# Kernel tuning notes

Hardware: AMD Instinct MI355X
Metric: run time of the kernel (lower is better)

Reference implementation:

```python
import jax, jax.numpy as jnp
import numpy as np

B, H, W, C = 32, 64, 64, 512
NUM_HEADS = 16
WS = 8          # window_size
SHIFT = 4       # shift_size = WS // 2
MLP_HIDDEN = 2048
N = WS * WS     # tokens per window
NW = (H // WS) * (W // WS)  # windows per image


def _rel_coords_table():
    # Swin-V2 log-spaced continuous relative coordinates, (1, 2*WS-1, 2*WS-1, 2)
    r = np.arange(-(WS - 1), WS, dtype=np.float32)
    t = np.stack(np.meshgrid(r, r, indexing='ij'), axis=-1)[None]
    t = t / (WS - 1) * 8.0
    t = np.sign(t) * np.log2(np.abs(t) + 1.0) / np.log2(8.0)
    return t.astype(np.float32)


def _rel_pos_index():
    coords = np.stack(np.meshgrid(np.arange(WS), np.arange(WS), indexing='ij'))
    cf = coords.reshape(2, -1)
    rel = (cf[:, :, None] - cf[:, None, :]).transpose(1, 2, 0)
    rel[..., 0] += WS - 1
    rel[..., 1] += WS - 1
    rel[..., 0] *= 2 * WS - 1
    return rel.sum(-1)  # (N, N) int


def _attn_mask():
    # shifted-window mask: -100 where tokens come from different image regions
    img = np.zeros((H, W), np.float32)
    cnt = 0
    for hs in (slice(0, -WS), slice(-WS, -SHIFT), slice(-SHIFT, None)):
        for ws_ in (slice(0, -WS), slice(-WS, -SHIFT), slice(-SHIFT, None)):
            img[hs, ws_] = cnt
            cnt += 1
    mw = img.reshape(H // WS, WS, W // WS, WS).transpose(0, 2, 1, 3).reshape(-1, N)
    diff = mw[:, None, :] - mw[:, :, None]
    return np.where(diff != 0, np.float32(-100.0), np.float32(0.0))  # (NW, N, N)


_RCT = jnp.asarray(_rel_coords_table())
_RPI = jnp.asarray(_rel_pos_index().reshape(-1))
_MASK = jnp.asarray(_attn_mask())
_LOGIT_MAX = float(np.log(1.0 / 0.01))


def _layernorm(x, w, b):
    mu = x.mean(-1, keepdims=True)
    var = ((x - mu) ** 2).mean(-1, keepdims=True)
    return (x - mu) / jnp.sqrt(var + 1e-5) * w + b


def setup_inputs() -> dict:
    key = jax.random.key(0)
    ks = jax.random.split(key, 8)
    s = 0.02
    return {
        'x': jax.random.normal(ks[0], (B, H * W, C), jnp.float32),
        'qkv_w': jax.random.normal(ks[1], (3 * C, C), jnp.float32) * s,
        'q_bias': jnp.zeros((C,), jnp.float32),
        'v_bias': jnp.zeros((C,), jnp.float32),
        'logit_scale': jnp.log(10.0 * jnp.ones((NUM_HEADS, 1, 1), jnp.float32)),
        'cpb_w1': jax.random.normal(ks[2], (512, 2), jnp.float32) * s,
        'cpb_b1': jnp.zeros((512,), jnp.float32),
        'cpb_w2': jax.random.normal(ks[3], (NUM_HEADS, 512), jnp.float32) * s,
        'proj_w': jax.random.normal(ks[4], (C, C), jnp.float32) * s,
        'proj_b': jnp.zeros((C,), jnp.float32),
        'norm1_w': jnp.ones((C,), jnp.float32),
        'norm1_b': jnp.zeros((C,), jnp.float32),
        'norm2_w': jnp.ones((C,), jnp.float32),
        'norm2_b': jnp.zeros((C,), jnp.float32),
        'fc1_w': jax.random.normal(ks[5], (MLP_HIDDEN, C), jnp.float32) * s,
        'fc1_b': jnp.zeros((MLP_HIDDEN,), jnp.float32),
        'fc2_w': jax.random.normal(ks[6], (C, MLP_HIDDEN), jnp.float32) * s,
        'fc2_b': jnp.zeros((C,), jnp.float32),
    }


def reference(x, qkv_w, q_bias, v_bias, logit_scale, cpb_w1, cpb_b1, cpb_w2,
              proj_w, proj_b, norm1_w, norm1_b, norm2_w, norm2_b,
              fc1_w, fc1_b, fc2_w, fc2_b):
    hd = C // NUM_HEADS
    shortcut = x
    xi = x.reshape(B, H, W, C)
    xi = jnp.roll(xi, shift=(-SHIFT, -SHIFT), axis=(1, 2))
    # window partition -> (B*NW, N, C)
    xw = xi.reshape(B, H // WS, WS, W // WS, WS, C).transpose(0, 1, 3, 2, 4, 5).reshape(-1, N, C)
    # qkv with q/v bias only (k bias = 0), Swin-V2 style
    qkv_b = jnp.concatenate([q_bias, jnp.zeros_like(v_bias), v_bias])
    qkv = (xw @ qkv_w.T + qkv_b).reshape(-1, N, 3, NUM_HEADS, hd).transpose(2, 0, 3, 1, 4)
    q, k, v = qkv[0], qkv[1], qkv[2]  # (B_, nH, N, hd)
    # cosine attention
    qn = q / jnp.maximum(jnp.linalg.norm(q, axis=-1, keepdims=True), 1e-12)
    kn = k / jnp.maximum(jnp.linalg.norm(k, axis=-1, keepdims=True), 1e-12)
    attn = jnp.einsum('whnd,whmd->whnm', qn, kn)
    scale = jnp.exp(jnp.minimum(logit_scale, _LOGIT_MAX))  # (nH,1,1)
    attn = attn * scale
    # continuous relative position bias via small MLP
    table = (jax.nn.relu(_RCT @ cpb_w1.T + cpb_b1) @ cpb_w2.T).reshape(-1, NUM_HEADS)
    bias = table[_RPI].reshape(N, N, NUM_HEADS).transpose(2, 0, 1)  # (nH, N, N)
    bias = 16.0 * jax.nn.sigmoid(bias)
    attn = attn + bias[None]
    # shift mask
    attn = attn.reshape(B, NW, NUM_HEADS, N, N) + _MASK[None, :, None]
    attn = jax.nn.softmax(attn.reshape(-1, NUM_HEADS, N, N), axis=-1)
    out = jnp.einsum('whnm,whmd->whnd', attn, v).transpose(0, 2, 1, 3).reshape(-1, N, C)
    out = out @ proj_w.T + proj_b
    # window reverse + un-shift
    xi = out.reshape(B, H // WS, W // WS, WS, WS, C).transpose(0, 1, 3, 2, 4, 5).reshape(B, H, W, C)
    xi = jnp.roll(xi, shift=(SHIFT, SHIFT), axis=(1, 2)).reshape(B, H * W, C)
    # Swin-V2 post-norm residuals
    x = shortcut + _layernorm(xi, norm1_w, norm1_b)
    h = jax.nn.gelu(x @ fc1_w.T + fc1_b, approximate=False)
    y = h @ fc2_w.T + fc2_b
    x = x + _layernorm(y, norm2_w, norm2_b)
    return x
```

## Files before the change

kernel.cpp:

```cpp
#include <hip/hip_runtime.h>

typedef unsigned short u16;
typedef unsigned int u32;
typedef __attribute__((ext_vector_type(8))) __bf16 bf16x8;
typedef __attribute__((ext_vector_type(8))) short s16x8;
typedef __attribute__((ext_vector_type(4))) short s16x4;
typedef __attribute__((ext_vector_type(4))) float f32x4;

static __device__ __forceinline__ float bf2f(u16 h){
  union{u32 u; float f;} v; v.u = ((u32)h)<<16; return v.f;
}
static __device__ __forceinline__ u16 cvtbf(float f){
  return __builtin_bit_cast(u16, (__bf16)f);
}

#define GLD16(gp, lp) __builtin_amdgcn_global_load_lds(                      \
  (__attribute__((address_space(1))) void*)(void*)(gp),                      \
  (__attribute__((address_space(3))) void*)(void*)(lp), 16, 0, 0)

__global__ __launch_bounds__(256)
void prep_x_kernel(const float* __restrict__ x, u16* __restrict__ xw)
{
  const int t = threadIdx.x, wv = t>>6, ln = t&63;
  const size_t row = (size_t)blockIdx.x*4 + wv;
  const int b = (int)(row>>12), wl = (int)((row>>6)&63), m = (int)(row&63);
  const int gh = ((wl>>3)*8 + (m>>3) + 4) & 63;
  const int gw = ((wl&7)*8 + (m&7) + 4) & 63;
  const size_t src = ((size_t)b*4096 + (size_t)gh*64 + gw)*512 + (size_t)ln*8;
  f32x4 a = *(const f32x4*)&x[src];
  f32x4 c = *(const f32x4*)&x[src+4];
  s16x8 o;
#pragma unroll
  for (int j=0;j<4;j++){ o[j] = (short)cvtbf(a[j]); o[j+4] = (short)cvtbf(c[j]); }
  *(s16x8*)&xw[row*512 + (size_t)ln*8] = o;
}

__global__ __launch_bounds__(256)
void cvt_bf16_kernel(const float* __restrict__ src, u16* __restrict__ dst, int n)
{
  const int i = (blockIdx.x*256 + threadIdx.x)*8;
  if (i >= n) return;
  f32x4 a = *(const f32x4*)&src[i];
  f32x4 c = *(const f32x4*)&src[i+4];
  s16x8 o;
#pragma unroll
  for (int j=0;j<4;j++){ o[j] = (short)cvtbf(a[j]); o[j+4] = (short)cvtbf(c[j]); }
  *(s16x8*)&dst[i] = o;
}

static __device__ __forceinline__ float logcoord(int d){
  const float tt = (float)d * (8.0f/7.0f);
  const float sg = (tt > 0.f) ? 1.f : ((tt < 0.f) ? -1.f : 0.f);
  return sg * log2f(fabsf(tt) + 1.f) * (1.f/3.f);
}

__global__ __launch_bounds__(512)
void cpb_table_kernel(const float* __restrict__ w1, const float* __restrict__ b1,
                      const float* __restrict__ w2, float* __restrict__ table)
{
  __shared__ float hid[512];
  const int r = blockIdx.x, j = threadIdx.x;
  const float va = logcoord(r/15 - 7);
  const float vb = logcoord(r%15 - 7);
  hid[j] = fmaxf(va*w1[2*j] + vb*w1[2*j+1] + b1[j], 0.f);
  __syncthreads();
  if (j < 16){
    float acc = 0.f;
    for (int i=0;i<512;i++) acc += hid[i]*w2[j*512+i];
    table[r*16 + j] = acc;
  }
}

__global__ __launch_bounds__(256)
void bias_expand_kernel(const float* __restrict__ table, float* __restrict__ biasT)
{
  const int gid = blockIdx.x*256 + threadIdx.x;
  const int h = gid>>12, ij = gid&4095, i = ij>>6, j = ij&63;
  const int dr = (i>>3)-(j>>3)+7, dc = (i&7)-(j&7)+7;
  const float v = table[(dr*15+dc)*16 + h];
  biasT[gid] = 16.f / (1.f + __expf(-v));
}

template<int EPI>
__global__ __launch_bounds__(512, 4)
void gemm128(const u16* __restrict__ A, const u16* __restrict__ B,
             u16* __restrict__ Co, const float* __restrict__ bias0,
             const float* __restrict__ bias1, int N, int K)
{
  extern __shared__ u16 ls[];
  const int t = threadIdx.x;
  const int wv = t>>6, ln = t&63;
  const int wr = wv>>2, wc = wv&3;
  const int lr = ln&15, lg = ln>>4;
  const int gx = gridDim.x;
  const int lin = blockIdx.y*gx + blockIdx.x;
  const int q = (gx*(int)gridDim.y)>>3;
  const int lin2 = (lin&7)*q + (lin>>3);
  const int mT = lin2/gx, nT = lin2 - mT*gx;

  const int rSub = ln>>2;
  const int cS = ((ln&3) ^ ((ln>>3)&3)) * 8;
  const u16* gA = A + (size_t)(mT*128 + wv*16 + rSub)*K + cS;
  const u16* gB = B + (size_t)(nT*256 + wv*16 + rSub)*K + cS;
  const size_t rstepB = (size_t)128*K;
  char* lA = (char*)ls + wv*1024;

  const int cR = (lg ^ ((lr>>1)&3))*8;
  const int offA0 = (wr*64 + lr)*32 + cR;
  const int offB0 = (wc*64 + lr)*32 + cR;

#define STAGE(buf, tt) do {                                                  \
    char* p_ = lA + (buf)*24576;                                             \
    const size_t ko_ = (size_t)(tt)*32;                                      \
    GLD16(gA + ko_,          p_);                                            \
    GLD16(gB + ko_,          p_ + 8192);                                     \
    GLD16(gB + ko_ + rstepB, p_ + 16384);                                    \
  } while(0)

  f32x4 acc[4][4] = {};

#define COMPUTE(buf) do {                                                    \
    const u16* la_ = ls + (buf)*12288;                                       \
    const u16* lb_ = la_ + 4096;                                             \
    bf16x8 bfr[4];                                                           \
    _Pragma("unroll")                                                        \
    for (int nt=0;nt<4;nt++) bfr[nt] = *(const bf16x8*)&lb_[offB0 + nt*512]; \
    _Pragma("unroll")                                                        \
    for (int mt=0;mt<4;mt++){                                                \
      bf16x8 af = *(const bf16x8*)&la_[offA0 + mt*512];                      \
      _Pragma("unroll")                                                      \
      for (int nt=0;nt<4;nt++)                                               \
        acc[mt][nt] = __builtin_amdgcn_mfma_f32_16x16x32_bf16(af, bfr[nt], acc[mt][nt], 0,0,0); \
    }                                                                        \
  } while(0)

  const int nsteps = K>>5;
  STAGE(0,0); STAGE(1,1);
  int cb = 0;
  for (int t_=0; t_<nsteps-1; ++t_){
    asm volatile("s_waitcnt vmcnt(3)\n\ts_barrier" ::: "memory");
    if (t_+2 < nsteps){
      int sb = cb+2; if (sb>=3) sb-=3;
      STAGE(sb, t_+2);
    }
    COMPUTE(cb);
    cb = (cb==2)?0:cb+1;
  }
  asm volatile("s_waitcnt vmcnt(0)\n\ts_barrier" ::: "memory");
  COMPUTE(cb);
#undef STAGE
#undef COMPUTE

  if (EPI == 0) {
    const int cb0 = nT*256 + wc*64;
    int secA[4], hhA[4], dA[4]; float bbA[4];
#pragma unroll
    for (int nt=0; nt<4; nt++) {
      const int cbp = cb0 + nt*16;
      secA[nt] = cbp >> 9;
      hhA[nt]  = (cbp >> 5) & 15;
      dA[nt]   = (cbp & 16) + lr;
      bbA[nt]  = (secA[nt]==1) ? 0.f : ((secA[nt]==0)?bias0:bias1)[(hhA[nt]<<5)+dA[nt]];
    }
#pragma unroll
    for (int mt=0; mt<4; mt++) {
      const int row = mT*128 + wr*64 + mt*16 + lg*4;
      const int win = row>>6, tok0 = row&63;
#pragma unroll
      for (int rr=0; rr<4; rr++) {
#pragma unroll
        for (int nt=0; nt<4; nt++) {
          u16* p = Co + (size_t)secA[nt]*67108864ULL + (size_t)win*32768
                      + hhA[nt]*2048 + (tok0+rr)*32 + dA[nt];
          *p = cvtbf(acc[mt][nt][rr] + bbA[nt]);
        }
      }
    }
  } else {
    const int c0 = nT*256 + wc*64;
    const int r0 = mT*128 + wr*64 + lg*4;
    float bbA[4];
#pragma unroll
    for (int nt=0; nt<4; nt++) bbA[nt] = bias0[c0 + nt*16 + lr];
#pragma unroll
    for (int mt=0; mt<4; mt++) {
#pragma unroll
      for (int rr=0; rr<4; rr++) {
        u16* pr = Co + (size_t)(r0 + mt*16 + rr)*N + c0 + lr;
#pragma unroll
        for (int nt=0; nt<4; nt++) {
          float v = acc[mt][nt][rr] + bbA[nt];
          if (EPI == 2) {
            const float z = 1.5957691216f * v * fmaf(0.044715f, v*v, 1.0f);
            v = v * __builtin_amdgcn_rcpf(1.0f + __expf(-z));
          }
          pr[nt*16] = cvtbf(v);
        }
      }
    }
  }
}

__global__ __launch_bounds__(256)
void attn_win(const u16* __restrict__ qkv, const float* __restrict__ biasT,
              const float* __restrict__ logit_scale, u16* __restrict__ aout)
{
  __shared__ float sb[4096];
  __shared__ u16 sp[4][4096];
  __shared__ u16 svt[4][2048];
  const int t = threadIdx.x, wv = t>>6, ln = t&63;
  const int lr = ln&15, lg = ln>>4;
  const int head = blockIdx.y;
  for (int i = t; i < 4096; i += 256) sb[i] = biasT[head*4096 + i];
  __syncthreads();
  const int win = blockIdx.x*4 + wv;
  const size_t whi = (size_t)win*16 + head;
  const u16* qb = qkv + whi*2048;
  const u16* kb = qkv + 67108864ULL + whi*2048;
  const u16* vb = qkv + 134217728ULL + whi*2048;

  s16x8 qs[4], ks[4];
  float qin[4], kin[4];
#pragma unroll
  for (int mt=0;mt<4;mt++){
    qs[mt] = *(const s16x8*)&qb[(mt*16+lr)*32 + lg*8];
    float ss = 0.f;
#pragma unroll
    for (int j=0;j<8;j++){ float f = bf2f((u16)qs[mt][j]); ss += f*f; }
    ss += __shfl_xor(ss, 16); ss += __shfl_xor(ss, 32);
    qin[mt] = 1.f / fmaxf(sqrtf(ss), 1e-12f);
  }
#pragma unroll
  for (int nt=0;nt<4;nt++){
    ks[nt] = *(const s16x8*)&kb[(nt*16+lr)*32 + lg*8];
    float ss = 0.f;
#pragma unroll
    for (int j=0;j<8;j++){ float f = bf2f((u16)ks[nt][j]); ss += f*f; }
    ss += __shfl_xor(ss, 16); ss += __shfl_xor(ss, 32);
    kin[nt] = 1.f / fmaxf(sqrtf(ss), 1e-12f);
  }
  f32x4 S[4][4] = {};
#pragma unroll
  for (int mt=0;mt<4;mt++)
#pragma unroll
    for (int nt=0;nt<4;nt++)
      S[mt][nt] = __builtin_amdgcn_mfma_f32_16x16x32_bf16(
          __builtin_bit_cast(bf16x8, qs[mt]), __builtin_bit_cast(bf16x8, ks[nt]),
          S[mt][nt], 0,0,0);

  const float scale = expf(fminf(logit_scale[head], 4.6051702f));
  const int wl = win & 63, wh = wl>>3, ww = wl&7;
  float rsum[4][4];
#pragma unroll
  for (int mt=0;mt<4;mt++){
#pragma unroll
    for (int rr=0;rr<4;rr++){
      const int msub = lg*4 + rr;
      const float qn = __shfl(qin[mt], msub);
      const int m = mt*16 + msub;
      const int ridm = (wh==7 ? (((m>>3)<4) ? 3 : 6) : 0) + (ww==7 ? (((m&7)<4) ? 1 : 2) : 0);
#pragma unroll
      for (int nt=0;nt<4;nt++){
        const int n = nt*16 + lr;
        const int ridn = (wh==7 ? (((n>>3)<4) ? 3 : 6) : 0) + (ww==7 ? (((n&7)<4) ? 1 : 2) : 0);
        float v = S[mt][nt][rr] * (qn * kin[nt] * scale) + sb[m*64+n];
        if (ridm != ridn) v -= 100.f;
        S[mt][nt][rr] = v;
      }
      float mx = fmaxf(fmaxf(S[mt][0][rr], S[mt][1][rr]), fmaxf(S[mt][2][rr], S[mt][3][rr]));
      mx = fmaxf(mx, __shfl_xor(mx, 1)); mx = fmaxf(mx, __shfl_xor(mx, 2));
      mx = fmaxf(mx, __shfl_xor(mx, 4)); mx = fmaxf(mx, __shfl_xor(mx, 8));
      float sm = 0.f;
#pragma unroll
      for (int nt=0;nt<4;nt++){ float p = __expf(S[mt][nt][rr]-mx); S[mt][nt][rr] = p; sm += p; }
      sm += __shfl_xor(sm,1); sm += __shfl_xor(sm,2); sm += __shfl_xor(sm,4); sm += __shfl_xor(sm,8);
      rsum[mt][rr] = sm;
#pragma unroll
      for (int nt=0;nt<4;nt++){
        const int n = nt*16 + lr;
        sp[wv][(m*64 + n) ^ ((m&7)<<3)] = cvtbf(S[mt][nt][rr]);
      }
    }
  }
#pragma unroll
  for (int it=0; it<8; it++){
    const int flat = it*256 + ln*4;
    const int k = flat>>5, d0 = flat&31;
    s16x4 vv = *(const s16x4*)&vb[k*32 + d0];
#pragma unroll
    for (int e=0;e<4;e++)
      svt[wv][((d0+e)*64 + k) ^ (((d0+e)&7)<<3)] = (u16)vv[e];
  }
  f32x4 O[4][2] = {};
#pragma unroll
  for (int kk=0; kk<2; kk++){
    bf16x8 pf[4], vf[2];
#pragma unroll
    for (int mt=0;mt<4;mt++){
      const int am = mt*16 + lr;
      const int idx = (am*64 + kk*32 + lg*8) ^ ((am&7)<<3);
      s16x8 tmp; __builtin_memcpy(&tmp, (const char*)&sp[wv][0] + 2*idx, 16);
      pf[mt] = __builtin_bit_cast(bf16x8, tmp);
    }
#pragma unroll
    for (int n2=0;n2<2;n2++){
      const int vn = n2*16 + lr;
      const int idx = (vn*64 + kk*32 + lg*8) ^ ((vn&7)<<3);
      s16x8 tmp; __builtin_memcpy(&tmp, (const char*)&svt[wv][0] + 2*idx, 16);
      vf[n2] = __builtin_bit_cast(bf16x8, tmp);
    }
#pragma unroll
    for (int mt=0;mt<4;mt++)
#pragma unroll
      for (int n2=0;n2<2;n2++)
        O[mt][n2] = __builtin_amdgcn_mfma_f32_16x16x32_bf16(pf[mt], vf[n2], O[mt][n2], 0,0,0);
  }
  const size_t obase = (size_t)win*64;
#pragma unroll
  for (int mt=0;mt<4;mt++)
#pragma unroll
  for (int rr=0;rr<4;rr++){
    const int m = mt*16 + lg*4 + rr;
    const float inv = 1.f / rsum[mt][rr];
#pragma unroll
    for (int n2=0;n2<2;n2++){
      const int d = n2*16 + lr;
      aout[(obase + m)*512 + head*32 + d] = cvtbf(O[mt][n2][rr] * inv);
    }
  }
}

__global__ __launch_bounds__(256)
void scatter_ln_kernel(const u16* __restrict__ po, const float* __restrict__ x,
                       const float* __restrict__ w, const float* __restrict__ bb,
                       u16* __restrict__ x1b)
{
  const int t = threadIdx.x, wv = t>>6, ln = t&63;
  const size_t row = (size_t)blockIdx.x*4 + wv;
  s16x8 pv = *(const s16x8*)&po[row*512 + (size_t)ln*8];
  float v[8]; float s=0.f, s2=0.f;
#pragma unroll
  for (int j=0;j<8;j++){ v[j] = bf2f((u16)pv[j]); s += v[j]; s2 += v[j]*v[j]; }
#pragma unroll
  for (int d=1; d<64; d<<=1){ s += __shfl_xor(s,d); s2 += __shfl_xor(s2,d); }
  const float mu = s * 0.001953125f;
  const float var = s2 * 0.001953125f - mu*mu;
  const float rs = rsqrtf(var + 1e-5f);
  const int b = (int)(row>>12), wl = (int)((row>>6)&63), m = (int)(row&63);
  const int gh = ((wl>>3)*8 + (m>>3) + 4) & 63;
  const int gw = ((wl&7)*8 + (m&7) + 4) & 63;
  const size_t img = ((size_t)b*4096 + (size_t)gh*64 + gw)*512 + (size_t)ln*8;
  f32x4 xa = *(const f32x4*)&x[img];
  f32x4 xc = *(const f32x4*)&x[img+4];
  s16x8 ob;
  const int c0 = ln*8;
#pragma unroll
  for (int j=0;j<8;j++){
    const int c = c0 + j;
    const float lnv = (v[j]-mu)*rs*w[c] + bb[c];
    const float xx = (j<4) ? xa[j] : xc[j-4];
    ob[j] = (short)cvtbf(xx + lnv);
  }
  *(s16x8*)&x1b[img] = ob;
}

__global__ __launch_bounds__(256)
void final_ln_kernel(const u16* __restrict__ y, const u16* __restrict__ x1b,
                     const float* __restrict__ w, const float* __restrict__ bb,
                     float* __restrict__ out)
{
  const int t = threadIdx.x, wv = t>>6, ln = t&63;
  const size_t row = (size_t)blockIdx.x*4 + wv;
  const size_t idx = row*512 + (size_t)ln*8;
  s16x8 yv = *(const s16x8*)&y[idx];
  float v[8]; float s=0.f, s2=0.f;
#pragma unroll
  for (int j=0;j<8;j++){ v[j] = bf2f((u16)yv[j]); s += v[j]; s2 += v[j]*v[j]; }
#pragma unroll
  for (int d=1; d<64; d<<=1){ s += __shfl_xor(s,d); s2 += __shfl_xor(s2,d); }
  const float mu = s * 0.001953125f;
  const float var = s2 * 0.001953125f - mu*mu;
  const float rs = rsqrtf(var + 1e-5f);
  s16x8 xv = *(const s16x8*)&x1b[idx];
  f32x4 oa, oc;
  const int c0 = ln*8;
#pragma unroll
  for (int j=0;j<8;j++){
    const int c = c0 + j;
    const float lnv = (v[j]-mu)*rs*w[c] + bb[c];
    const float o = bf2f((u16)xv[j]) + lnv;
    if (j<4) oa[j] = o; else oc[j-4] = o;
  }
  *(f32x4*)&out[idx] = oa;
  *(f32x4*)&out[idx+4] = oc;
}

extern "C" void kernel_launch(void* const* d_in, const int* in_sizes, int n_in,
                              void* d_out, int out_size, void* d_ws, size_t ws_size,
                              hipStream_t stream)
{
  (void)in_sizes; (void)n_in; (void)out_size; (void)ws_size;
  const float* x        = (const float*)d_in[0];
  const float* qkv_w    = (const float*)d_in[1];
  const float* q_bias   = (const float*)d_in[2];
  const float* v_bias   = (const float*)d_in[3];
  const float* lscale   = (const float*)d_in[4];
  const float* cpb_w1   = (const float*)d_in[5];
  const float* cpb_b1   = (const float*)d_in[6];
  const float* cpb_w2   = (const float*)d_in[7];
  const float* proj_w   = (const float*)d_in[8];
  const float* proj_b   = (const float*)d_in[9];
  const float* n1w      = (const float*)d_in[10];
  const float* n1b      = (const float*)d_in[11];
  const float* n2w      = (const float*)d_in[12];
  const float* n2b      = (const float*)d_in[13];
  const float* fc1_w    = (const float*)d_in[14];
  const float* fc1_b    = (const float*)d_in[15];
  const float* fc2_w    = (const float*)d_in[16];
  const float* fc2_b    = (const float*)d_in[17];

  char* ws = (char*)d_ws;
  constexpr size_t XW_OFF   = 0;
  constexpr size_t ATT_OFF  = 134217728ULL;
  constexpr size_t PRJ_OFF  = 268435456ULL;
  constexpr size_t H_OFF    = 0;
  constexpr size_t BIAS_OFF = 536870912ULL;
  constexpr size_t TAB_OFF  = BIAS_OFF + 262144;
  constexpr size_t WQKV_OFF = TAB_OFF + 16384;
  constexpr size_t WPRJ_OFF = WQKV_OFF + 1572864;
  constexpr size_t WFC1_OFF = WPRJ_OFF + 524288;
  constexpr size_t WFC2_OFF = WFC1_OFF + 2097152;
  constexpr size_t QKV_OFF  = WFC2_OFF + 2097152;
  constexpr size_t X1B_OFF  = QKV_OFF;
  constexpr size_t Y_OFF    = QKV_OFF + 134217728ULL;

  u16*   xw    = (u16*)(ws + XW_OFF);
  u16*   attnO = (u16*)(ws + ATT_OFF);
  u16*   projO = (u16*)(ws + PRJ_OFF);
  u16*   hbuf  = (u16*)(ws + H_OFF);
  float* biasT = (float*)(ws + BIAS_OFF);
  float* table = (float*)(ws + TAB_OFF);
  u16*   wqkv  = (u16*)(ws + WQKV_OFF);
  u16*   wprj  = (u16*)(ws + WPRJ_OFF);
  u16*   wfc1  = (u16*)(ws + WFC1_OFF);
  u16*   wfc2  = (u16*)(ws + WFC2_OFF);
  u16*   qkvB  = (u16*)(ws + QKV_OFF);
  u16*   x1b   = (u16*)(ws + X1B_OFF);
  u16*   ybuf  = (u16*)(ws + Y_OFF);

  hipFuncSetAttribute((const void*)gemm128<0>, hipFuncAttributeMaxDynamicSharedMemorySize, 73728);
  hipFuncSetAttribute((const void*)gemm128<1>, hipFuncAttributeMaxDynamicSharedMemorySize, 73728);
  hipFuncSetAttribute((const void*)gemm128<2>, hipFuncAttributeMaxDynamicSharedMemorySize, 73728);
  hipFuncSetAttribute((const void*)gemm128<3>, hipFuncAttributeMaxDynamicSharedMemorySize, 73728);

  cvt_bf16_kernel<<<384, 256, 0, stream>>>(qkv_w, wqkv, 786432);
  cvt_bf16_kernel<<<128, 256, 0, stream>>>(proj_w, wprj, 262144);
  cvt_bf16_kernel<<<512, 256, 0, stream>>>(fc1_w, wfc1, 1048576);
  cvt_bf16_kernel<<<512, 256, 0, stream>>>(fc2_w, wfc2, 1048576);
  prep_x_kernel<<<32768, 256, 0, stream>>>(x, xw);
  cpb_table_kernel<<<225, 512, 0, stream>>>(cpb_w1, cpb_b1, cpb_w2, table);
  bias_expand_kernel<<<256, 256, 0, stream>>>(table, biasT);
  gemm128<0><<<dim3(6,1024), 512, 73728, stream>>>(xw, wqkv, qkvB, q_bias, v_bias, 1536, 512);
  attn_win<<<dim3(512,16), 256, 0, stream>>>(qkvB, biasT, lscale, attnO);
  gemm128<1><<<dim3(2,1024), 512, 73728, stream>>>(attnO, wprj, projO, proj_b, nullptr, 512, 512);
  scatter_ln_kernel<<<32768, 256, 0, stream>>>(projO, x, n1w, n1b, x1b);
  gemm128<2><<<dim3(8,1024), 512, 73728, stream>>>(x1b, wfc1, hbuf, fc1_b, nullptr, 2048, 512);
  gemm128<3><<<dim3(2,1024), 512, 73728, stream>>>(hbuf, wfc2, ybuf, fc2_b, nullptr, 512, 2048);
  final_ln_kernel<<<32768, 256, 0, stream>>>(ybuf, x1b, n2w, n2b, (float*)d_out);
}
```

Baseline: 1.531 ms.

## Rewrite GEMMs as 256x256 tiles with eight-phase ping-pong pipeline

Replaces the 128x256-tile, triple-buffered GEMM with a 256x256-tile kernel that uses BK=64 split into two K halves. Each iteration runs eight phases that interleave LDS fragment reads, global-to-LDS staging, barriers and MFMA clusters raised with s_setprio. This is meant to raise arithmetic intensity per LDS byte and overlap loads with compute more tightly. In exchange it doubles the accumulators (128 fp32 per lane), cuts occupancy to 2 blocks with 128KB LDS, and halves the grid size.

```diff
diff --git a/kernel.cpp b/kernel.cpp
--- a/kernel.cpp
+++ b/kernel.cpp
@@ -82,10 +82,10 @@
 }
 
 template<int EPI>
-__global__ __launch_bounds__(512, 4)
-void gemm128(const u16* __restrict__ A, const u16* __restrict__ B,
-             u16* __restrict__ Co, const float* __restrict__ bias0,
-             const float* __restrict__ bias1, int N, int K)
+__global__ __launch_bounds__(512, 2)
+void gemm8p(const u16* __restrict__ A, const u16* __restrict__ B,
+            u16* __restrict__ Co, const float* __restrict__ bias0,
+            const float* __restrict__ bias1, int N, int K)
 {
   extern __shared__ u16 ls[];
   const int t = threadIdx.x;
@@ -98,58 +98,79 @@
   const int lin2 = (lin&7)*q + (lin>>3);
   const int mT = lin2/gx, nT = lin2 - mT*gx;
 
-  const int rSub = ln>>2;
   const int cS = ((ln&3) ^ ((ln>>3)&3)) * 8;
-  const u16* gA = A + (size_t)(mT*128 + wv*16 + rSub)*K + cS;
-  const u16* gB = B + (size_t)(nT*256 + wv*16 + rSub)*K + cS;
-  const size_t rstepB = (size_t)128*K;
-  char* lA = (char*)ls + wv*1024;
+  const u16* gA0 = A + (size_t)(mT*256 + wv*16 + (ln>>2))*K + cS;
+  const u16* gB0 = B + (size_t)(nT*256 + wv*16 + (ln>>2))*K + cS;
+  const size_t rstep = (size_t)128*K;
 
   const int cR = (lg ^ ((lr>>1)&3))*8;
-  const int offA0 = (wr*64 + lr)*32 + cR;
-  const int offB0 = (wc*64 + lr)*32 + cR;
-
-#define STAGE(buf, tt) do {                                                  \
-    char* p_ = lA + (buf)*24576;                                             \
-    const size_t ko_ = (size_t)(tt)*32;                                      \
-    GLD16(gA + ko_,          p_);                                            \
-    GLD16(gB + ko_,          p_ + 8192);                                     \
-    GLD16(gB + ko_ + rstepB, p_ + 16384);                                    \
+  const int rA = (wr*128 + lr)*32 + cR;
+  const int rB = 16384 + (wc*64 + lr)*32 + cR;
+
+#define STG(gbase, tau, kh, isB) do {                                        \
+    char* d_ = (char*)ls + (((tau)&1)*32768 + ((isB)?16384:0) + (kh)*8192 + wv*512)*2; \
+    const u16* s_ = (gbase) + (size_t)(tau)*64 + (kh)*32;                    \
+    GLD16(s_,         d_);                                                   \
+    GLD16(s_ + rstep, d_ + 8192);                                            \
   } while(0)
 
-  f32x4 acc[4][4] = {};
-
-#define COMPUTE(buf) do {                                                    \
-    const u16* la_ = ls + (buf)*12288;                                       \
-    const u16* lb_ = la_ + 4096;                                             \
-    bf16x8 bfr[4];                                                           \
+  f32x4 acc[8][4] = {};
+  bf16x8 bB[4];
+
+#define PH(d, ks, BNEW, mtg, STAGES, VM) do {                                \
+    const u16* la_ = ls + (d)*32768 + (ks)*8192;                             \
+    bf16x8 aF0 = *(const bf16x8*)&la_[rA + ((mtg)+0)*512];                   \
+    bf16x8 aF1 = *(const bf16x8*)&la_[rA + ((mtg)+1)*512];                   \
+    bf16x8 aF2 = *(const bf16x8*)&la_[rA + ((mtg)+2)*512];                   \
+    bf16x8 aF3 = *(const bf16x8*)&la_[rA + ((mtg)+3)*512];                   \
+    if (BNEW) {                                                              \
+      bB[0] = *(const bf16x8*)&la_[rB + 0*512];                              \
+      bB[1] = *(const bf16x8*)&la_[rB + 1*512];                              \
+      bB[2] = *(const bf16x8*)&la_[rB + 2*512];                              \
+      bB[3] = *(const bf16x8*)&la_[rB + 3*512];                              \
+    }                                                                        \
+    STAGES;                                                                  \
+    __builtin_amdgcn_s_barrier();                                            \
+    __builtin_amdgcn_s_setprio(1);                                           \
     _Pragma("unroll")                                                        \
-    for (int nt=0;nt<4;nt++) bfr[nt] = *(const bf16x8*)&lb_[offB0 + nt*512]; \
+    for (int nt=0;nt<4;nt++)                                                 \
+      acc[(mtg)+0][nt] = __builtin_amdgcn_mfma_f32_16x16x32_bf16(aF0, bB[nt], acc[(mtg)+0][nt], 0,0,0); \
     _Pragma("unroll")                                                        \
-    for (int mt=0;mt<4;mt++){                                                \
-      bf16x8 af = *(const bf16x8*)&la_[offA0 + mt*512];                      \
-      _Pragma("unroll")                                                      \
-      for (int nt=0;nt<4;nt++)                                               \
-        acc[mt][nt] = __builtin_amdgcn_mfma_f32_16x16x32_bf16(af, bfr[nt], acc[mt][nt], 0,0,0); \
-    }                                                                        \
+    for (int nt=0;nt<4;nt++)                                                 \
+      acc[(mtg)+1][nt] = __builtin_amdgcn_mfma_f32_16x16x32_bf16(aF1, bB[nt], acc[(mtg)+1][nt], 0,0,0); \
+    _Pragma("unroll")                                                        \
+    for (int nt=0;nt<4;nt++)                                                 \
+      acc[(mtg)+2][nt] = __builtin_amdgcn_mfma_f32_16x16x32_bf16(aF2, bB[nt], acc[(mtg)+2][nt], 0,0,0); \
+    _Pragma("unroll")                                                        \
+    for (int nt=0;nt<4;nt++)                                                 \
+      acc[(mtg)+3][nt] = __builtin_amdgcn_mfma_f32_16x16x32_bf16(aF3, bB[nt], acc[(mtg)+3][nt], 0,0,0); \
+    __builtin_amdgcn_s_setprio(0);                                           \
+    if (VM) asm volatile("s_waitcnt vmcnt(4)" ::: "memory");                 \
+    __builtin_amdgcn_s_barrier();                                            \
   } while(0)
 
-  const int nsteps = K>>5;
-  STAGE(0,0); STAGE(1,1);
-  int cb = 0;
-  for (int t_=0; t_<nsteps-1; ++t_){
-    asm volatile("s_waitcnt vmcnt(3)\n\ts_barrier" ::: "memory");
-    if (t_+2 < nsteps){
-      int sb = cb+2; if (sb>=3) sb-=3;
-      STAGE(sb, t_+2);
-    }
-    COMPUTE(cb);
-    cb = (cb==2)?0:cb+1;
-  }
-  asm volatile("s_waitcnt vmcnt(0)\n\ts_barrier" ::: "memory");
-  COMPUTE(cb);
-#undef STAGE
-#undef COMPUTE
+  const int ntk = K>>6;
+  const int niter = ntk>>1;
+  STG(gA0,0,0,0); STG(gB0,0,0,1);
+  STG(gA0,0,1,0); STG(gB0,0,1,1);
+  STG(gA0,1,0,0); STG(gB0,1,0,1);
+  asm volatile("s_waitcnt vmcnt(4)" ::: "memory");
+  __builtin_amdgcn_s_barrier();
+
+  for (int it=0; it<niter; ++it){
+    const int T = 2*it;
+    const bool s2 = (T+2) < ntk, s3 = (T+3) < ntk;
+    PH(0,0,1,0, { STG(gA0,T+1,1,0); STG(gB0,T+1,1,1); }, 0);
+    PH(0,0,0,4, {}, 0);
+    PH(0,1,1,0, { if(s2) STG(gA0,T+2,0,0); }, 0);
+    PH(0,1,0,4, { if(s2) STG(gB0,T+2,0,1); }, 1);
+    PH(1,0,1,0, { if(s2){ STG(gA0,T+2,1,0); STG(gB0,T+2,1,1);} }, 0);
+    PH(1,0,0,4, {}, 0);
+    PH(1,1,1,0, { if(s3) STG(gA0,T+3,0,0); }, 0);
+    PH(1,1,0,4, { if(s3) STG(gB0,T+3,0,1); }, 1);
+  }
+#undef PH
+#undef STG
 
   if (EPI == 0) {
     const int cb0 = nT*256 + wc*64;
@@ -163,8 +184,8 @@
       bbA[nt]  = (secA[nt]==1) ? 0.f : ((secA[nt]==0)?bias0:bias1)[(hhA[nt]<<5)+dA[nt]];
     }
 #pragma unroll
-    for (int mt=0; mt<4; mt++) {
-      const int row = mT*128 + wr*64 + mt*16 + lg*4;
+    for (int mt=0; mt<8; mt++) {
+      const int row = mT*256 + wr*128 + mt*16 + lg*4;
       const int win = row>>6, tok0 = row&63;
 #pragma unroll
       for (int rr=0; rr<4; rr++) {
@@ -178,12 +199,12 @@
     }
   } else {
     const int c0 = nT*256 + wc*64;
-    const int r0 = mT*128 + wr*64 + lg*4;
+    const int r0 = mT*256 + wr*128 + lg*4;
     float bbA[4];
 #pragma unroll
     for (int nt=0; nt<4; nt++) bbA[nt] = bias0[c0 + nt*16 + lr];
 #pragma unroll
-    for (int mt=0; mt<4; mt++) {
+    for (int mt=0; mt<8; mt++) {
 #pragma unroll
       for (int rr=0; rr<4; rr++) {
         u16* pr = Co + (size_t)(r0 + mt*16 + rr)*N + c0 + lr;
@@ -448,10 +469,10 @@
   u16*   x1b   = (u16*)(ws + X1B_OFF);
   u16*   ybuf  = (u16*)(ws + Y_OFF);
 
-  hipFuncSetAttribute((const void*)gemm128<0>, hipFuncAttributeMaxDynamicSharedMemorySize, 73728);
-  hipFuncSetAttribute((const void*)gemm128<1>, hipFuncAttributeMaxDynamicSharedMemorySize, 73728);
-  hipFuncSetAttribute((const void*)gemm128<2>, hipFuncAttributeMaxDynamicSharedMemorySize, 73728);
-  hipFuncSetAttribute((const void*)gemm128<3>, hipFuncAttributeMaxDynamicSharedMemorySize, 73728);
+  hipFuncSetAttribute((const void*)gemm8p<0>, hipFuncAttributeMaxDynamicSharedMemorySize, 131072);
+  hipFuncSetAttribute((const void*)gemm8p<1>, hipFuncAttributeMaxDynamicSharedMemorySize, 131072);
+  hipFuncSetAttribute((const void*)gemm8p<2>, hipFuncAttributeMaxDynamicSharedMemorySize, 131072);
+  hipFuncSetAttribute((const void*)gemm8p<3>, hipFuncAttributeMaxDynamicSharedMemorySize, 131072);
 
   cvt_bf16_kernel<<<384, 256, 0, stream>>>(qkv_w, wqkv, 786432);
   cvt_bf16_kernel<<<128, 256, 0, stream>>>(proj_w, wprj, 262144);
@@ -460,11 +481,11 @@
   prep_x_kernel<<<32768, 256, 0, stream>>>(x, xw);
   cpb_table_kernel<<<225, 512, 0, stream>>>(cpb_w1, cpb_b1, cpb_w2, table);
   bias_expand_kernel<<<256, 256, 0, stream>>>(table, biasT);
-  gemm128<0><<<dim3(6,1024), 512, 73728, stream>>>(xw, wqkv, qkvB, q_bias, v_bias, 1536, 512);
+  gemm8p<0><<<dim3(6,512), 512, 131072, stream>>>(xw, wqkv, qkvB, q_bias, v_bias, 1536, 512);
   attn_win<<<dim3(512,16), 256, 0, stream>>>(qkvB, biasT, lscale, attnO);
-  gemm128<1><<<dim3(2,1024), 512, 73728, stream>>>(attnO, wprj, projO, proj_b, nullptr, 512, 512);
+  gemm8p<1><<<dim3(2,512), 512, 131072, stream>>>(attnO, wprj, projO, proj_b, nullptr, 512, 512);
   scatter_ln_kernel<<<32768, 256, 0, stream>>>(projO, x, n1w, n1b, x1b);
-  gemm128<2><<<dim3(8,1024), 512, 73728, stream>>>(x1b, wfc1, hbuf, fc1_b, nullptr, 2048, 512);
-  gemm128<3><<<dim3(2,1024), 512, 73728, stream>>>(hbuf, wfc2, ybuf, fc2_b, nullptr, 512, 2048);
+  gemm8p<2><<<dim3(8,512), 512, 131072, stream>>>(x1b, wfc1, hbuf, fc1_b, nullptr, 2048, 512);
+  gemm8p<3><<<dim3(2,512), 512, 131072, stream>>>(hbuf, wfc2, ybuf, fc2_b, nullptr, 512, 2048);
   final_ln_kernel<<<32768, 256, 0, stream>>>(ybuf, x1b, n2w, n2b, (float*)d_out);
 }
```

New measurement: 1.582 ms. 3.3% more time.
